# Performance work log

Hardware: AMD Instinct MI355X
Metric: run time of the kernel (lower is better)

## Reference

```python
import jax, jax.numpy as jnp
import numpy as np

N1 = 100000  # source cloud size (x1)
N2 = 100000  # target cloud size (x2)
F = 64       # point feature dim
E = 1600000  # number of radius edges (avg 16 neighbors)
H = 128      # MLP hidden/out dim


def setup_inputs() -> dict:
    key = jax.random.key(0)
    ks = jax.random.split(key, 12)
    s = 0.05
    return {
        "x1_features": jax.random.normal(ks[0], (N1, F), jnp.float32),
        "x1_pos": jax.random.normal(ks[1], (N1, 3), jnp.float32),
        "x2_features": jax.random.normal(ks[2], (N2, F), jnp.float32),
        "x2_pos": jax.random.normal(ks[3], (N2, 3), jnp.float32),
        "W1": jax.random.normal(ks[4], (2 * F + 3, H), jnp.float32) * s,
        "b1": jnp.zeros((H,), jnp.float32),
        "W2": jax.random.normal(ks[5], (H, H), jnp.float32) * s,
        "b2": jnp.zeros((H,), jnp.float32),
        "W3": jax.random.normal(ks[6], (H, H), jnp.float32) * s,
        "b3": jnp.zeros((H,), jnp.float32),
        "edge_src": jax.random.randint(ks[7], (E,), 0, N1, jnp.int32),
        "edge_dst": jax.random.randint(ks[8], (E,), 0, N2, jnp.int32),
    }


def reference(x1_features, x1_pos, x2_features, x2_pos,
              W1, b1, W2, b2, W3, b3, edge_src, edge_dst):
    # message(x_i, x_j, pos_i, pos_j): i = target (x2, edge_dst), j = source (x1, edge_src)
    # msg = cat([x_i, x_j, pos_j - pos_i], dim=1)  -> [E, 2F+3]
    msg = jnp.concatenate(
        [x2_features[edge_dst],
         x1_features[edge_src],
         x1_pos[edge_src] - x2_pos[edge_dst]], axis=1)
    # MLP (Linear+ReLU x3, FastFlow3D make_mlp style)
    h = jax.nn.relu(msg @ W1 + b1)
    h = jax.nn.relu(h @ W2 + b2)
    h = jax.nn.relu(h @ W3 + b3)
    # scatter-max aggregation onto x2 nodes; PyG fills empty segments with 0
    out = jax.ops.segment_max(h, edge_dst, num_segments=N2)
    out = jnp.where(jnp.isneginf(out), 0.0, out)
    return out, x2_pos
```

## Files before the change

kernel.cpp:

```cpp
#include <hip/hip_runtime.h>
#include <hip/hip_bf16.h>

#define DEV __device__ __forceinline__

typedef short bf16x8 __attribute__((ext_vector_type(8)));
typedef float f32x16 __attribute__((ext_vector_type(16)));

static constexpr int FDIM  = 64;
static constexpr int HH    = 128;
static constexpr int K1RAW = 2 * FDIM + 3;
static constexpr int K1    = 144;
static constexpr int KS1   = K1 / 16;
static constexpr int KS2   = HH / 16;
static constexpr int TM    = 128;

static constexpr int CSTR  = TM * 16 + 16;
static constexpr int MCH   = 18;
static constexpr int HCH   = 16;
static constexpr int L_MSG = 0;
static constexpr int L_H   = MCH * CSTR;
static constexpr int L_DST = L_H + HCH * CSTR;
static constexpr int L_TOT = L_DST + TM * 4;

static constexpr int WT1_ELEMS = HH * K1;
static constexpr int WT2_ELEMS = HH * HH;
static constexpr int WT_TOTAL  = WT1_ELEMS + 2 * WT2_ELEMS;

DEV unsigned pack2(float a, float b) {
    union { __hip_bfloat162 h; unsigned u; } cv;
    cv.h.x = __float2bfloat16(a);
    cv.h.y = __float2bfloat16(b);
    return cv.u;
}
DEV unsigned short f2bf(float f) {
    union { __hip_bfloat16 h; unsigned short u; } cv;
    cv.h = __float2bfloat16(f);
    return cv.u;
}

__global__ void k_cvt(const float* __restrict__ src, unsigned short* __restrict__ dst, int n8) {
    int i = blockIdx.x * 256 + threadIdx.x;
    if (i < n8) {
        float4 a = *(const float4*)(src + (size_t)i * 8);
        float4 b = *(const float4*)(src + (size_t)i * 8 + 4);
        uint4 o;
        o.x = pack2(a.x, a.y); o.y = pack2(a.z, a.w);
        o.z = pack2(b.x, b.y); o.w = pack2(b.z, b.w);
        *(uint4*)(dst + (size_t)i * 8) = o;
    }
}

__global__ void k_wprep(const float* __restrict__ W1, const float* __restrict__ W2,
                        const float* __restrict__ W3, unsigned short* __restrict__ wt) {
    int i = blockIdx.x * 256 + threadIdx.x;
    if (i < WT1_ELEMS) {
        int n = i / K1, k = i % K1;
        float v = (k < K1RAW) ? W1[k * HH + n] : 0.f;
        wt[i] = f2bf(v);
    } else if (i < WT1_ELEMS + WT2_ELEMS) {
        int j = i - WT1_ELEMS; int n = j / HH, k = j % HH;
        wt[i] = f2bf(W2[k * HH + n]);
    } else if (i < WT_TOTAL) {
        int j = i - WT1_ELEMS - WT2_ELEMS; int n = j / HH, k = j % HH;
        wt[i] = f2bf(W3[k * HH + n]);
    }
}

__global__ void k_hist(const int* __restrict__ edst, int* __restrict__ cnt, int E) {
    int e = blockIdx.x * 256 + threadIdx.x;
    if (e < E) atomicAdd(&cnt[edst[e]], 1);
}

__global__ void k_scan_part(const int* __restrict__ cnt, int* __restrict__ partial, int n2) {
    __shared__ int sm[256];
    int t = threadIdx.x;
    int base = blockIdx.x * 1024 + t * 4;
    int s = 0;
#pragma unroll
    for (int j = 0; j < 4; j++) { int idx = base + j; if (idx < n2) s += cnt[idx]; }
    sm[t] = s; __syncthreads();
    for (int off = 128; off > 0; off >>= 1) {
        if (t < off) sm[t] += sm[t + off];
        __syncthreads();
    }
    if (t == 0) partial[blockIdx.x] = sm[0];
}

__global__ void k_scan_top(int* __restrict__ partial, int nb) {
    __shared__ int sm[256];
    int t = threadIdx.x;
    int v = (t < nb) ? partial[t] : 0;
    sm[t] = v; __syncthreads();
    for (int off = 1; off < 256; off <<= 1) {
        int add = (t >= off) ? sm[t - off] : 0;
        __syncthreads();
        sm[t] += add;
        __syncthreads();
    }
    if (t < nb) partial[t] = sm[t] - v;
}

__global__ void k_scan_down(const int* __restrict__ cnt, const int* __restrict__ partial,
                            int* __restrict__ cursor, int n2) {
    __shared__ int sm[256];
    int t = threadIdx.x;
    int base = blockIdx.x * 1024 + t * 4;
    int c[4]; int s = 0;
#pragma unroll
    for (int j = 0; j < 4; j++) { int idx = base + j; c[j] = (idx < n2) ? cnt[idx] : 0; s += c[j]; }
    sm[t] = s; __syncthreads();
    for (int off = 1; off < 256; off <<= 1) {
        int add = (t >= off) ? sm[t - off] : 0;
        __syncthreads();
        sm[t] += add;
        __syncthreads();
    }
    int run = partial[blockIdx.x] + (sm[t] - s);
#pragma unroll
    for (int j = 0; j < 4; j++) {
        int idx = base + j;
        if (idx < n2) cursor[idx] = run;
        run += c[j];
    }
}

__global__ void k_fill(const int* __restrict__ edst, int* __restrict__ cursor,
                       int* __restrict__ csr_e, int* __restrict__ csr_d, int E) {
    int e = blockIdx.x * 256 + threadIdx.x;
    if (e < E) {
        int d = edst[e];
        int p = atomicAdd(&cursor[d], 1);
        csr_e[p] = e;
        csr_d[p] = d;
    }
}

DEV f32x16 zerov() {
    f32x16 v;
#pragma unroll
    for (int i = 0; i < 16; i++) v[i] = 0.f;
    return v;
}

template <int KSTEPS>
DEV void load_A(const unsigned short* __restrict__ wtl, int rt, int l31, int hh, bf16x8* A) {
#pragma unroll
    for (int ks = 0; ks < KSTEPS; ks++)
        A[ks] = *(const bf16x8*)(wtl + (rt * 32 + l31) * (KSTEPS * 16) + ks * 16 + 8 * hh);
}

template <int KSTEPS>
DEV f32x16 tile_mfma(const bf16x8* A, const char* __restrict__ srcrow) {
    f32x16 acc = zerov();
#pragma unroll
    for (int ks = 0; ks < KSTEPS; ks++) {
        bf16x8 B = *(const bf16x8*)(srcrow + 2 * ks * CSTR);
        acc = __builtin_amdgcn_mfma_f32_32x32x16_bf16(A[ks], B, acc, 0, 0, 0);
    }
    return acc;
}

DEV void tile_store(const f32x16& acc, const float* __restrict__ bias, char* __restrict__ dstrow,
                    int rt, int hh) {
#pragma unroll
    for (int g = 0; g < 4; g++) {
        float4 bv = *(const float4*)(bias + rt * 32 + 8 * g + 4 * hh);
        float v0 = fmaxf(acc[4 * g + 0] + bv.x, 0.f);
        float v1 = fmaxf(acc[4 * g + 1] + bv.y, 0.f);
        float v2 = fmaxf(acc[4 * g + 2] + bv.z, 0.f);
        float v3 = fmaxf(acc[4 * g + 3] + bv.w, 0.f);
        uint2 w; w.x = pack2(v0, v1); w.y = pack2(v2, v3);
        *(uint2*)(dstrow + g * CSTR) = w;
    }
}

template <bool SORTED, bool BF16SRC>
__global__ __launch_bounds__(512, 4) void k_main(
    const float* __restrict__ x1f, const float* __restrict__ x1p,
    const float* __restrict__ x2f, const float* __restrict__ x2p,
    const char* __restrict__ xb1, const char* __restrict__ xb2,
    const float* __restrict__ b1, const float* __restrict__ b2, const float* __restrict__ b3,
    const unsigned short* __restrict__ wt,
    const int* __restrict__ csr_e, const int* __restrict__ csr_d,
    const int* __restrict__ edge_src, const int* __restrict__ edge_dst,
    float* __restrict__ out, int E) {
    __shared__ __align__(16) char sm[L_TOT];
    char* msg = sm + L_MSG;
    char* hbf = sm + L_H;
    int*  dl  = (int*)(sm + L_DST);

    const int tid  = threadIdx.x;
    const int lane = tid & 63;
    const int wv   = tid >> 6;
    const int l31  = lane & 31;
    const int hh   = lane >> 5;
    const int eb   = blockIdx.x * TM;

    {
        const int r   = tid >> 2;
        const int sub = tid & 3;
        const int slot = eb + r;
        const bool ok = slot < E;
        int e = 0, d = 0, s = 0;
        if (ok) {
            if (SORTED) { e = csr_e[slot]; d = csr_d[slot]; }
            else        { e = slot;        d = edge_dst[e]; }
            s = edge_src[e];
        }
        if (sub == 0) dl[r] = ok ? d : -1;
        char* colbase = msg + r * 16 + (sub * 4) * CSTR;
#pragma unroll
        for (int i = 0; i < 4; i++) {
            const int c = sub * 4 + i;
            uint4 v; v.x = v.y = v.z = v.w = 0u;
            if (ok) {
                const int cc = c & 7;
                if (BF16SRC) {
                    const char* base = (c < 8) ? (xb2 + (size_t)d * (2 * FDIM))
                                               : (xb1 + (size_t)s * (2 * FDIM));
                    v = *(const uint4*)(base + cc * 16);
                } else {
                    const float* base = (c < 8) ? (x2f + (size_t)d * FDIM)
                                                : (x1f + (size_t)s * FDIM);
                    float4 a = *(const float4*)(base + cc * 8);
                    float4 b = *(const float4*)(base + cc * 8 + 4);
                    v.x = pack2(a.x, a.y); v.y = pack2(a.z, a.w);
                    v.z = pack2(b.x, b.y); v.w = pack2(b.z, b.w);
                }
            }
            *(uint4*)(colbase + i * CSTR) = v;
        }
        if (sub == 3) {
            float dx = 0.f, dy = 0.f, dz = 0.f;
            if (ok) {
                dx = x1p[s * 3 + 0] - x2p[d * 3 + 0];
                dy = x1p[s * 3 + 1] - x2p[d * 3 + 1];
                dz = x1p[s * 3 + 2] - x2p[d * 3 + 2];
            }
            char* rowb = msg + r * 16;
            uint4 v; v.x = pack2(dx, dy); v.y = pack2(dz, 0.f); v.z = 0u; v.w = 0u;
            *(uint4*)(rowb + 16 * CSTR) = v;
            uint4 z; z.x = z.y = z.z = z.w = 0u;
            *(uint4*)(rowb + 17 * CSTR) = z;
        }
    }
    __syncthreads();

    const int rt  = wv & 3;
    const int ct0 = (wv >> 2) * 2;
    bf16x8 A[KS1];

    load_A<KS1>(wt, rt, l31, hh, A);
#pragma unroll
    for (int j = 0; j < 2; j++) {
        const int r = (ct0 + j) * 32 + l31;
        f32x16 acc = tile_mfma<KS1>(A, msg + r * 16 + hh * CSTR);
        tile_store(acc, b1, hbf + r * 16 + 8 * hh + (4 * rt) * CSTR, rt, hh);
    }
    __syncthreads();

    load_A<KS2>(wt + WT1_ELEMS, rt, l31, hh, A);
#pragma unroll
    for (int j = 0; j < 2; j++) {
        const int r = (ct0 + j) * 32 + l31;
        f32x16 acc = tile_mfma<KS2>(A, hbf + r * 16 + hh * CSTR);
        tile_store(acc, b2, msg + r * 16 + 8 * hh + (4 * rt) * CSTR, rt, hh);
    }
    __syncthreads();

    load_A<KS2>(wt + WT1_ELEMS + WT2_ELEMS, rt, l31, hh, A);
#pragma unroll
    for (int j = 0; j < 2; j++) {
        const int r = (ct0 + j) * 32 + l31;
        f32x16 acc = tile_mfma<KS2>(A, msg + r * 16 + hh * CSTR);
        tile_store(acc, b3, hbf + r * 16 + 8 * hh + (4 * rt) * CSTR, rt, hh);
    }
    __syncthreads();

    {
        const int p     = tid & 63;
        const int strip = tid >> 6;
        const int r0 = strip * 16;
        const char* fbase = hbf + (p >> 2) * CSTR + (p & 3) * 4;
        int curd = dl[r0];
        int rs = r0;
        float m0 = 0.f, m1 = 0.f;
#pragma unroll
        for (int r = r0; r < r0 + 16; r++) {
            int d = dl[r];
            if (d != curd) {
                if (curd >= 0) {
                    bool extL = (rs == r0) && (r0 == 0 || dl[r0 - 1] == curd);
                    if (extL) {
                        if (m0 > 0.f) atomicMax((int*)out + (size_t)curd * HH + 2 * p,     __float_as_int(m0));
                        if (m1 > 0.f) atomicMax((int*)out + (size_t)curd * HH + 2 * p + 1, __float_as_int(m1));
                    } else {
                        out[(size_t)curd * HH + 2 * p]     = m0;
                        out[(size_t)curd * HH + 2 * p + 1] = m1;
                    }
                }
                curd = d; rs = r; m0 = 0.f; m1 = 0.f;
            }
            unsigned w = *(const unsigned*)(fbase + r * 16);
            m0 = fmaxf(m0, __uint_as_float(w << 16));
            m1 = fmaxf(m1, __uint_as_float(w & 0xffff0000u));
        }
        if (curd >= 0) {
            bool extL = (rs == r0) && (r0 == 0 || dl[r0 - 1] == curd);
            bool extR = (r0 + 16 == TM) || (dl[r0 + 16] == curd);
            if (extL || extR) {
                if (m0 > 0.f) atomicMax((int*)out + (size_t)curd * HH + 2 * p,     __float_as_int(m0));
                if (m1 > 0.f) atomicMax((int*)out + (size_t)curd * HH + 2 * p + 1, __float_as_int(m1));
            } else {
                out[(size_t)curd * HH + 2 * p]     = m0;
                out[(size_t)curd * HH + 2 * p + 1] = m1;
            }
        }
    }
}

extern "C" void kernel_launch(void* const* d_in, const int* in_sizes, int n_in,
                              void* d_out, int out_size, void* d_ws, size_t ws_size,
                              hipStream_t stream) {
    const float* x1f = (const float*)d_in[0];
    const float* x1p = (const float*)d_in[1];
    const float* x2f = (const float*)d_in[2];
    const float* x2p = (const float*)d_in[3];
    const float* W1  = (const float*)d_in[4];
    const float* b1  = (const float*)d_in[5];
    const float* W2  = (const float*)d_in[6];
    const float* b2  = (const float*)d_in[7];
    const float* W3  = (const float*)d_in[8];
    const float* b3  = (const float*)d_in[9];
    const int* esrc  = (const int*)d_in[10];
    const int* edst  = (const int*)d_in[11];
    const int E  = in_sizes[10];
    const int N1 = in_sizes[1] / 3;
    const int N2 = in_sizes[3] / 3;
    float* out = (float*)d_out;

    size_t off = 0;
    auto take = [&](size_t bytes) { size_t o = off; off = (off + bytes + 255) & ~(size_t)255; return o; };
    size_t o_cnt = take(4 * (size_t)N2);
    size_t o_cur = take(4 * (size_t)N2);
    size_t o_par = take(4 * 256);
    size_t o_ce  = take(4 * (size_t)E);
    size_t o_cd  = take(4 * (size_t)E);
    size_t o_wt  = take(2 * (size_t)WT_TOTAL);
    size_t need_csr = off;
    size_t o_x1  = take(2 * (size_t)N1 * FDIM);
    size_t o_x2  = take(2 * (size_t)N2 * FDIM);
    size_t need_bf = off;

    const int NB = (N2 + 1023) / 1024;
    bool use_csr = (need_csr <= ws_size) && (NB <= 256);
    bool use_bf  = (need_bf <= ws_size);

    char* ws = (char*)d_ws;
    unsigned short* wt = use_csr ? (unsigned short*)(ws + o_wt) : (unsigned short*)ws;
    int* cnt    = (int*)(ws + o_cnt);
    int* cursor = (int*)(ws + o_cur);
    int* part   = (int*)(ws + o_par);
    int* csr_e  = (int*)(ws + o_ce);
    int* csr_d  = (int*)(ws + o_cd);
    char* xb1   = ws + o_x1;
    char* xb2   = ws + o_x2;

    (void)hipMemsetAsync(out, 0, (size_t)N2 * HH * 4, stream);
    (void)hipMemcpyAsync(out + (size_t)N2 * HH, x2p, (size_t)N2 * 3 * 4,
                         hipMemcpyDeviceToDevice, stream);

    k_wprep<<<(WT_TOTAL + 255) / 256, 256, 0, stream>>>(W1, W2, W3, wt);

    if (use_bf) {
        int n8_1 = N1 * FDIM / 8, n8_2 = N2 * FDIM / 8;
        k_cvt<<<(n8_1 + 255) / 256, 256, 0, stream>>>(x1f, (unsigned short*)xb1, n8_1);
        k_cvt<<<(n8_2 + 255) / 256, 256, 0, stream>>>(x2f, (unsigned short*)xb2, n8_2);
    }

    const int grid = (E + TM - 1) / TM;
    if (use_csr) {
        (void)hipMemsetAsync(cnt, 0, 4 * (size_t)N2, stream);
        k_hist<<<(E + 255) / 256, 256, 0, stream>>>(edst, cnt, E);
        k_scan_part<<<NB, 256, 0, stream>>>(cnt, part, N2);
        k_scan_top<<<1, 256, 0, stream>>>(part, NB);
        k_scan_down<<<NB, 256, 0, stream>>>(cnt, part, cursor, N2);
        k_fill<<<(E + 255) / 256, 256, 0, stream>>>(edst, cursor, csr_e, csr_d, E);
        if (use_bf)
            k_main<true, true><<<grid, 512, 0, stream>>>(
                x1f, x1p, x2f, x2p, xb1, xb2, b1, b2, b3, wt, csr_e, csr_d, esrc, edst, out, E);
        else
            k_main<true, false><<<grid, 512, 0, stream>>>(
                x1f, x1p, x2f, x2p, xb1, xb2, b1, b2, b3, wt, csr_e, csr_d, esrc, edst, out, E);
    } else {
        if (use_bf)
            k_main<false, true><<<grid, 512, 0, stream>>>(
                x1f, x1p, x2f, x2p, xb1, xb2, b1, b2, b3, wt, edst, edst, esrc, edst, out, E);
        else
            k_main<false, false><<<grid, 512, 0, stream>>>(
                x1f, x1p, x2f, x2p, xb1, xb2, b1, b2, b3, wt, edst, edst, esrc, edst, out, E);
    }
}
```

Before: 597.9 us.

## Gather layer-1 MFMA operands straight into registers and store source ids in CSR

```diff
diff --git a/kernel.cpp b/kernel.cpp
--- a/kernel.cpp
+++ b/kernel.cpp
@@ -15,12 +15,9 @@
 static constexpr int TM    = 128;
 
 static constexpr int CSTR  = TM * 16 + 16;
-static constexpr int MCH   = 18;
 static constexpr int HCH   = 16;
-static constexpr int L_MSG = 0;
-static constexpr int L_H   = MCH * CSTR;
-static constexpr int L_DST = L_H + HCH * CSTR;
-static constexpr int L_TOT = L_DST + TM * 4;
+static constexpr int HBUF  = HCH * CSTR;
+static constexpr int L_TOT = 2 * HBUF + TM * 4;
 
 static constexpr int WT1_ELEMS = HH * K1;
 static constexpr int WT2_ELEMS = HH * HH;
@@ -124,13 +121,14 @@
     }
 }
 
-__global__ void k_fill(const int* __restrict__ edst, int* __restrict__ cursor,
-                       int* __restrict__ csr_e, int* __restrict__ csr_d, int E) {
+__global__ void k_fill(const int* __restrict__ edst, const int* __restrict__ esrc,
+                       int* __restrict__ cursor,
+                       int* __restrict__ csr_s, int* __restrict__ csr_d, int E) {
     int e = blockIdx.x * 256 + threadIdx.x;
     if (e < E) {
         int d = edst[e];
         int p = atomicAdd(&cursor[d], 1);
-        csr_e[p] = e;
+        csr_s[p] = esrc[e];
         csr_d[p] = d;
     }
 }
@@ -181,13 +179,13 @@
     const char* __restrict__ xb1, const char* __restrict__ xb2,
     const float* __restrict__ b1, const float* __restrict__ b2, const float* __restrict__ b3,
     const unsigned short* __restrict__ wt,
-    const int* __restrict__ csr_e, const int* __restrict__ csr_d,
+    const int* __restrict__ csr_s, const int* __restrict__ csr_d,
     const int* __restrict__ edge_src, const int* __restrict__ edge_dst,
     float* __restrict__ out, int E) {
     __shared__ __align__(16) char sm[L_TOT];
-    char* msg = sm + L_MSG;
-    char* hbf = sm + L_H;
-    int*  dl  = (int*)(sm + L_DST);
+    char* hA = sm;
+    char* hB = sm + HBUF;
+    int*  dl = (int*)(sm + 2 * HBUF);
 
     const int tid  = threadIdx.x;
     const int lane = tid & 63;
@@ -196,84 +194,87 @@
     const int hh   = lane >> 5;
     const int eb   = blockIdx.x * TM;
 
-    {
-        const int r   = tid >> 2;
-        const int sub = tid & 3;
+    if (tid < TM) {
+        const int slot = eb + tid;
+        dl[tid] = (slot < E) ? (SORTED ? csr_d[slot] : edge_dst[slot]) : -1;
+    }
+
+    const int rt  = wv & 3;
+    const int ct0 = (wv >> 2) * 2;
+    bf16x8 A[KS1];
+
+    load_A<KS1>(wt, rt, l31, hh, A);
+#pragma unroll
+    for (int j = 0; j < 2; j++) {
+        const int r = (ct0 + j) * 32 + l31;
         const int slot = eb + r;
         const bool ok = slot < E;
-        int e = 0, d = 0, s = 0;
+        int d = 0, s = 0;
         if (ok) {
-            if (SORTED) { e = csr_e[slot]; d = csr_d[slot]; }
-            else        { e = slot;        d = edge_dst[e]; }
-            s = edge_src[e];
+            d = SORTED ? csr_d[slot] : edge_dst[slot];
+            s = SORTED ? csr_s[slot] : edge_src[slot];
         }
-        if (sub == 0) dl[r] = ok ? d : -1;
-        char* colbase = msg + r * 16 + (sub * 4) * CSTR;
-#pragma unroll
-        for (int i = 0; i < 4; i++) {
-            const int c = sub * 4 + i;
-            uint4 v; v.x = v.y = v.z = v.w = 0u;
-            if (ok) {
-                const int cc = c & 7;
-                if (BF16SRC) {
-                    const char* base = (c < 8) ? (xb2 + (size_t)d * (2 * FDIM))
-                                               : (xb1 + (size_t)s * (2 * FDIM));
-                    v = *(const uint4*)(base + cc * 16);
-                } else {
-                    const float* base = (c < 8) ? (x2f + (size_t)d * FDIM)
-                                                : (x1f + (size_t)s * FDIM);
-                    float4 a = *(const float4*)(base + cc * 8);
-                    float4 b = *(const float4*)(base + cc * 8 + 4);
-                    v.x = pack2(a.x, a.y); v.y = pack2(a.z, a.w);
-                    v.z = pack2(b.x, b.y); v.w = pack2(b.z, b.w);
-                }
+        bf16x8 Bv[KS1];
+        if (BF16SRC) {
+            const char* bx2 = xb2 + (size_t)d * (2 * FDIM);
+            const char* bx1 = xb1 + (size_t)s * (2 * FDIM);
+#pragma unroll
+            for (int ks = 0; ks < 4; ks++)
+                Bv[ks] = *(const bf16x8*)(bx2 + (2 * ks + hh) * 16);
+#pragma unroll
+            for (int ks = 4; ks < 8; ks++)
+                Bv[ks] = *(const bf16x8*)(bx1 + (2 * ks + hh) * 16 - 128);
+        } else {
+            const float* fx2 = x2f + (size_t)d * FDIM;
+            const float* fx1 = x1f + (size_t)s * FDIM;
+#pragma unroll
+            for (int ks = 0; ks < 8; ks++) {
+                const float* b = (ks < 4) ? (fx2 + (2 * ks + hh) * 8)
+                                          : (fx1 + (2 * ks + hh) * 8 - 64);
+                float4 a0 = *(const float4*)(b);
+                float4 a1 = *(const float4*)(b + 4);
+                union { unsigned u[4]; bf16x8 v; } B;
+                B.u[0] = pack2(a0.x, a0.y); B.u[1] = pack2(a0.z, a0.w);
+                B.u[2] = pack2(a1.x, a1.y); B.u[3] = pack2(a1.z, a1.w);
+                Bv[ks] = B.v;
             }
-            *(uint4*)(colbase + i * CSTR) = v;
         }
-        if (sub == 3) {
+        {
             float dx = 0.f, dy = 0.f, dz = 0.f;
             if (ok) {
                 dx = x1p[s * 3 + 0] - x2p[d * 3 + 0];
                 dy = x1p[s * 3 + 1] - x2p[d * 3 + 1];
                 dz = x1p[s * 3 + 2] - x2p[d * 3 + 2];
             }
-            char* rowb = msg + r * 16;
-            uint4 v; v.x = pack2(dx, dy); v.y = pack2(dz, 0.f); v.z = 0u; v.w = 0u;
-            *(uint4*)(rowb + 16 * CSTR) = v;
-            uint4 z; z.x = z.y = z.z = z.w = 0u;
-            *(uint4*)(rowb + 17 * CSTR) = z;
+            union { unsigned u[4]; bf16x8 v; } P;
+            P.u[0] = hh ? 0u : pack2(dx, dy);
+            P.u[1] = hh ? 0u : pack2(dz, 0.f);
+            P.u[2] = 0u; P.u[3] = 0u;
+            Bv[8] = P.v;
         }
+        f32x16 acc = zerov();
+#pragma unroll
+        for (int ks = 0; ks < KS1; ks++)
+            acc = __builtin_amdgcn_mfma_f32_32x32x16_bf16(A[ks], Bv[ks], acc, 0, 0, 0);
+        tile_store(acc, b1, hA + r * 16 + 8 * hh + (4 * rt) * CSTR, rt, hh);
     }
     __syncthreads();
 
-    const int rt  = wv & 3;
-    const int ct0 = (wv >> 2) * 2;
-    bf16x8 A[KS1];
-
-    load_A<KS1>(wt, rt, l31, hh, A);
+    load_A<KS2>(wt + WT1_ELEMS, rt, l31, hh, A);
 #pragma unroll
     for (int j = 0; j < 2; j++) {
         const int r = (ct0 + j) * 32 + l31;
-        f32x16 acc = tile_mfma<KS1>(A, msg + r * 16 + hh * CSTR);
-        tile_store(acc, b1, hbf + r * 16 + 8 * hh + (4 * rt) * CSTR, rt, hh);
+        f32x16 acc = tile_mfma<KS2>(A, hA + r * 16 + hh * CSTR);
+        tile_store(acc, b2, hB + r * 16 + 8 * hh + (4 * rt) * CSTR, rt, hh);
     }
     __syncthreads();
 
-    load_A<KS2>(wt + WT1_ELEMS, rt, l31, hh, A);
+    load_A<KS2>(wt + WT1_ELEMS + WT2_ELEMS, rt, l31, hh, A);
 #pragma unroll
     for (int j = 0; j < 2; j++) {
         const int r = (ct0 + j) * 32 + l31;
-        f32x16 acc = tile_mfma<KS2>(A, hbf + r * 16 + hh * CSTR);
-        tile_store(acc, b2, msg + r * 16 + 8 * hh + (4 * rt) * CSTR, rt, hh);
-    }
-    __syncthreads();
-
-    load_A<KS2>(wt + WT1_ELEMS + WT2_ELEMS, rt, l31, hh, A);
-#pragma unroll
-    for (int j = 0; j < 2; j++) {
-        const int r = (ct0 + j) * 32 + l31;
-        f32x16 acc = tile_mfma<KS2>(A, msg + r * 16 + hh * CSTR);
-        tile_store(acc, b3, hbf + r * 16 + 8 * hh + (4 * rt) * CSTR, rt, hh);
+        f32x16 acc = tile_mfma<KS2>(A, hB + r * 16 + hh * CSTR);
+        tile_store(acc, b3, hA + r * 16 + 8 * hh + (4 * rt) * CSTR, rt, hh);
     }
     __syncthreads();
 
@@ -281,7 +282,7 @@
         const int p     = tid & 63;
         const int strip = tid >> 6;
         const int r0 = strip * 16;
-        const char* fbase = hbf + (p >> 2) * CSTR + (p & 3) * 4;
+        const char* fbase = hA + (p >> 2) * CSTR + (p & 3) * 4;
         int curd = dl[r0];
         int rs = r0;
         float m0 = 0.f, m1 = 0.f;
@@ -344,7 +345,7 @@
     size_t o_cnt = take(4 * (size_t)N2);
     size_t o_cur = take(4 * (size_t)N2);
     size_t o_par = take(4 * 256);
-    size_t o_ce  = take(4 * (size_t)E);
+    size_t o_cs  = take(4 * (size_t)E);
     size_t o_cd  = take(4 * (size_t)E);
     size_t o_wt  = take(2 * (size_t)WT_TOTAL);
     size_t need_csr = off;
@@ -361,7 +362,7 @@
     int* cnt    = (int*)(ws + o_cnt);
     int* cursor = (int*)(ws + o_cur);
     int* part   = (int*)(ws + o_par);
-    int* csr_e  = (int*)(ws + o_ce);
+    int* csr_s  = (int*)(ws + o_cs);
     int* csr_d  = (int*)(ws + o_cd);
     char* xb1   = ws + o_x1;
     char* xb2   = ws + o_x2;
@@ -385,13 +386,13 @@
         k_scan_part<<<NB, 256, 0, stream>>>(cnt, part, N2);
         k_scan_top<<<1, 256, 0, stream>>>(part, NB);
         k_scan_down<<<NB, 256, 0, stream>>>(cnt, part, cursor, N2);
-        k_fill<<<(E + 255) / 256, 256, 0, stream>>>(edst, cursor, csr_e, csr_d, E);
+        k_fill<<<(E + 255) / 256, 256, 0, stream>>>(edst, esrc, cursor, csr_s, csr_d, E);
         if (use_bf)
             k_main<true, true><<<grid, 512, 0, stream>>>(
-                x1f, x1p, x2f, x2p, xb1, xb2, b1, b2, b3, wt, csr_e, csr_d, esrc, edst, out, E);
+                x1f, x1p, x2f, x2p, xb1, xb2, b1, b2, b3, wt, csr_s, csr_d, esrc, edst, out, E);
         else
             k_main<true, false><<<grid, 512, 0, stream>>>(
-                x1f, x1p, x2f, x2p, xb1, xb2, b1, b2, b3, wt, csr_e, csr_d, esrc, edst, out, E);
+                x1f, x1p, x2f, x2p, xb1, xb2, b1, b2, b3, wt, csr_s, csr_d, esrc, edst, out, E);
     } else {
         if (use_bf)
             k_main<false, true><<<grid, 512, 0, stream>>>(
```

After: 664.5 us. 11.1% more time.
